# Kernel optimization log

Hardware: AMD Instinct MI355X
Metric: run time of the kernel (lower is better)

Reference implementation:

```python
import jax, jax.numpy as jnp
import numpy as np

B, S, D = 4, 2048, 2048   # batch, seq, embed
E, R = 64, 64             # experts, expert_rank
INIT_SCALE = 0.02


def setup_inputs() -> dict:
    key = jax.random.key(0)
    k_x, k_m, k_up, k_dn = jax.random.split(key, 4)
    x = jax.random.normal(k_x, (B, S, D), dtype=jnp.float32)
    expert_mask = jax.random.uniform(k_m, (B, S, E), dtype=jnp.float32)
    # up_proj weight, out_first=True: [experts, rank, embed]
    w_up = jax.random.normal(k_up, (E, R, D), dtype=jnp.float32) * INIT_SCALE
    # down_proj weight, out_first=True: [embed, experts, rank]
    w_down = jax.random.normal(k_dn, (D, E, R), dtype=jnp.float32) * INIT_SCALE
    return {"x": x, "expert_mask": expert_mask, "w_up": w_up, "w_down": w_down}


def reference(x, expert_mask, w_up, w_down):
    # up projection: [B,S,D] x [E,R,D] -> [B,S,E,R]
    h = jnp.einsum("bsd,erd->bser", x, w_up)
    h = jax.nn.silu(h)
    # mask inactive experts (broadcast over rank)
    h = h * expert_mask[:, :, :, None]
    # down projection: [B,S,E,R] x [D,E,R] -> [B,S,D]
    out = jnp.einsum("bser,der->bsd", h, w_down)
    return out
```

## Files before the change

### kernel.cpp

```cpp
#include <hip/hip_runtime.h>
#include <hip/hip_bf16.h>

typedef unsigned short u16;
typedef unsigned int   u32;
typedef __attribute__((ext_vector_type(8))) short  s16x8;
typedef __attribute__((ext_vector_type(4))) float  f32x4;
typedef __attribute__((ext_vector_type(4))) unsigned short u16x4;

#define MT    8192
#define DE    2048
#define NEXP  64
#define ERDIM 4096

__device__ __forceinline__ u16 to_bf16(float f) {
  u32 u = __builtin_bit_cast(u32, f);
  u32 r = u + 0x7fffu + ((u >> 16) & 1u);
  return (u16)(r >> 16);
}

__global__ void cvt_f32_bf16(const float* __restrict__ in, u16* __restrict__ out, int n) {
  const int stride = gridDim.x * blockDim.x;
  for (int i = blockIdx.x * blockDim.x + threadIdx.x; i * 4 < n; i += stride) {
    const float4 v = *reinterpret_cast<const float4*>(in + (size_t)i * 4);
    u16x4 o;
    o.x = to_bf16(v.x); o.y = to_bf16(v.y); o.z = to_bf16(v.z); o.w = to_bf16(v.w);
    *reinterpret_cast<u16x4*>(out + (size_t)i * 4) = o;
  }
}

#define GLDS(gp, lp) __builtin_amdgcn_global_load_lds(                        \
    (const __attribute__((address_space(1))) void*)(gp),                      \
    (__attribute__((address_space(3))) void*)(lp), 16, 0, 0)

#define BAR() do { asm volatile("" ::: "memory");                             \
                   __builtin_amdgcn_s_barrier();                              \
                   asm volatile("" ::: "memory"); } while (0)

template<int FUSE, int K>
__global__ __launch_bounds__(512, 4) void gemm_bt(
    const u16* __restrict__ A, const u16* __restrict__ Bm,
    const float* __restrict__ mask, void* __restrict__ Cout,
    const int M, const int N)
{
  constexpr int BM = 256, BN = 128, BK = 32;
  constexpr int NT = K / BK;
  constexpr int SLOT = 12288;
  __shared__ __align__(16) u16 lds[3 * SLOT];

  const int nbn = N / BN;
  const int nwg = (int)gridDim.x;
  const int cpx = nwg >> 3;
  const int bid = (int)blockIdx.x;
  const int swz = (bid & 7) * cpx + (bid >> 3);
  const int bm = (swz / nbn) * BM;
  const int bn = (swz % nbn) * BN;

  const int tid  = (int)threadIdx.x;
  const int lane = tid & 63;
  const int w    = tid >> 6;
  const int wr   = w >> 1;
  const int wc   = w & 1;

  const int fr = lane & 15;
  const int cp = (lane >> 4) ^ ((lane >> 1) & 3);

  const int r0 = w * 16 + (lane >> 2);
  const int cl = (lane & 3) ^ ((lane >> 3) & 3);
  const u16* aS0 = A  + (size_t)(bm + r0) * K + cl * 8;
  const u16* aS1 = A  + (size_t)(bm + r0 + 128) * K + cl * 8;
  const u16* bS0 = Bm + (size_t)(bn + r0) * K + cl * 8;
  const int d0 = w * 512;

  f32x4 acc[4][4] = {};

#pragma unroll
  for (int t = 0; t < 2; ++t) {
    u16* dst = lds + t * SLOT;
    GLDS(aS0 + t * BK, dst +        d0);
    GLDS(aS1 + t * BK, dst + 4096 + d0);
    GLDS(bS0 + t * BK, dst + 8192 + d0);
  }
  asm volatile("s_waitcnt vmcnt(3)" ::: "memory");
  BAR();

  int ro = 0;
  int so = 2 * SLOT;
#pragma unroll 3
  for (int t = 0; t < NT; ++t) {
    const u16* sA = lds + ro;
    const u16* sB = lds + ro + 8192;

    s16x8 afr[4], bfr[4];
#pragma unroll
    for (int m = 0; m < 4; ++m)
      afr[m] = *reinterpret_cast<const s16x8*>(
          &sA[(wr * 64 + m * 16 + fr) * 32 + cp * 8]);
#pragma unroll
    for (int n = 0; n < 4; ++n)
      bfr[n] = *reinterpret_cast<const s16x8*>(
          &sB[(wc * 64 + n * 16 + fr) * 32 + cp * 8]);

    if (t + 2 < NT) {
      u16* dst = lds + so;
      const size_t koff = (size_t)(t + 2) * BK;
      GLDS(aS0 + koff, dst +        d0);
      GLDS(aS1 + koff, dst + 4096 + d0);
      GLDS(bS0 + koff, dst + 8192 + d0);
    }

    __builtin_amdgcn_s_setprio(1);
#pragma unroll
    for (int m = 0; m < 4; ++m)
#pragma unroll
      for (int n = 0; n < 4; ++n)
        acc[m][n] = __builtin_amdgcn_mfma_f32_16x16x32_bf16(
            afr[m], bfr[n], acc[m][n], 0, 0, 0);
    __builtin_amdgcn_s_setprio(0);

    if (t + 2 < NT)      asm volatile("s_waitcnt vmcnt(3)" ::: "memory");
    else if (t + 1 < NT) asm volatile("s_waitcnt vmcnt(0)" ::: "memory");

    if (t + 1 < NT) BAR();

    ro = (ro == 2 * SLOT) ? 0 : ro + SLOT;
    so = (so == 2 * SLOT) ? 0 : so + SLOT;
  }

  const int rgrp = (lane >> 4) * 4;
  if (FUSE) {
    u16* H = (u16*)Cout;
    const int ew = (bn + wc * 64) >> 6;
#pragma unroll
    for (int m = 0; m < 4; ++m) {
#pragma unroll
      for (int j = 0; j < 4; ++j) {
        const int grow = bm + wr * 64 + m * 16 + rgrp + j;
        const float mv = mask[(size_t)grow * NEXP + ew];
#pragma unroll
        for (int n = 0; n < 4; ++n) {
          const int gcol = bn + wc * 64 + n * 16 + fr;
          float v = acc[m][n][j];
          v = v / (1.0f + __expf(-v));
          H[(size_t)grow * N + gcol] = to_bf16(v * mv);
        }
      }
    }
  } else {
    float* O = (float*)Cout;
#pragma unroll
    for (int m = 0; m < 4; ++m) {
#pragma unroll
      for (int j = 0; j < 4; ++j) {
        const int grow = bm + wr * 64 + m * 16 + rgrp + j;
#pragma unroll
        for (int n = 0; n < 4; ++n) {
          const int gcol = bn + wc * 64 + n * 16 + fr;
          O[(size_t)grow * N + gcol] = acc[m][n][j];
        }
      }
    }
  }
}

extern "C" void kernel_launch(void* const* d_in, const int* in_sizes, int n_in,
                              void* d_out, int out_size, void* d_ws, size_t ws_size,
                              hipStream_t stream) {
  const float* x     = (const float*)d_in[0];
  const float* emask = (const float*)d_in[1];
  const float* w_up  = (const float*)d_in[2];
  const float* w_dn  = (const float*)d_in[3];
  float* out = (float*)d_out;

  const size_t need = ((size_t)MT * DE + (size_t)ERDIM * DE + (size_t)DE * ERDIM +
                       (size_t)MT * ERDIM) * sizeof(u16);
  if (ws_size < need) return;

  u16* xb  = (u16*)d_ws;
  u16* wub = xb  + (size_t)MT * DE;
  u16* wdb = wub + (size_t)ERDIM * DE;
  u16* hb  = wdb + (size_t)DE * ERDIM;

  hipLaunchKernelGGL(cvt_f32_bf16, dim3(2048), dim3(256), 0, stream, x,    xb,  MT * DE);
  hipLaunchKernelGGL(cvt_f32_bf16, dim3(1024), dim3(256), 0, stream, w_up, wub, ERDIM * DE);
  hipLaunchKernelGGL(cvt_f32_bf16, dim3(1024), dim3(256), 0, stream, w_dn, wdb, DE * ERDIM);

  hipLaunchKernelGGL((gemm_bt<1, DE>), dim3((MT / 256) * (ERDIM / 128)), dim3(512), 0, stream,
                     xb, wub, emask, (void*)hb, MT, ERDIM);
  hipLaunchKernelGGL((gemm_bt<0, ERDIM>), dim3((MT / 256) * (DE / 128)), dim3(512), 0, stream,
                     hb, wdb, nullptr, (void*)out, MT, DE);
}
```

Baseline: 311.2 us.

## Enlarge GEMM tiles to 256x256 with 1024 threads and 4-stage LDS pipeline

```diff
diff --git a/kernel.cpp b/kernel.cpp
--- a/kernel.cpp
+++ b/kernel.cpp
@@ -18,14 +18,23 @@
   return (u16)(r >> 16);
 }
 
-__global__ void cvt_f32_bf16(const float* __restrict__ in, u16* __restrict__ out, int n) {
+__global__ void cvt_all(const float* __restrict__ x,  u16* __restrict__ xo,
+                        const float* __restrict__ wu, u16* __restrict__ wuo,
+                        const float* __restrict__ wd, u16* __restrict__ wdo) {
   const int stride = gridDim.x * blockDim.x;
-  for (int i = blockIdx.x * blockDim.x + threadIdx.x; i * 4 < n; i += stride) {
-    const float4 v = *reinterpret_cast<const float4*>(in + (size_t)i * 4);
-    u16x4 o;
-    o.x = to_bf16(v.x); o.y = to_bf16(v.y); o.z = to_bf16(v.z); o.w = to_bf16(v.w);
-    *reinterpret_cast<u16x4*>(out + (size_t)i * 4) = o;
+  const int t0 = blockIdx.x * blockDim.x + threadIdx.x;
+#define CVT_LOOP(src, dst, nq)                                                \
+  for (int i = t0; i < (nq); i += stride) {                                   \
+    const float4 v = *reinterpret_cast<const float4*>((src) + (size_t)i * 4); \
+    u16x4 o;                                                                  \
+    o.x = to_bf16(v.x); o.y = to_bf16(v.y);                                   \
+    o.z = to_bf16(v.z); o.w = to_bf16(v.w);                                   \
+    *reinterpret_cast<u16x4*>((dst) + (size_t)i * 4) = o;                     \
   }
+  CVT_LOOP(x,  xo,  (MT * DE) / 4)
+  CVT_LOOP(wu, wuo, (ERDIM * DE) / 4)
+  CVT_LOOP(wd, wdo, (DE * ERDIM) / 4)
+#undef CVT_LOOP
 }
 
 #define GLDS(gp, lp) __builtin_amdgcn_global_load_lds(                        \
@@ -37,76 +46,68 @@
                    asm volatile("" ::: "memory"); } while (0)
 
 template<int FUSE, int K>
-__global__ __launch_bounds__(512, 4) void gemm_bt(
+__global__ __launch_bounds__(1024, 4) void gemm_bt(
     const u16* __restrict__ A, const u16* __restrict__ Bm,
     const float* __restrict__ mask, void* __restrict__ Cout,
     const int M, const int N)
 {
-  constexpr int BM = 256, BN = 128, BK = 32;
+  constexpr int BK = 32;
   constexpr int NT = K / BK;
-  constexpr int SLOT = 12288;
-  __shared__ __align__(16) u16 lds[3 * SLOT];
+  constexpr int SLOT = 16384;
+  __shared__ __align__(16) u16 lds[4 * SLOT];
 
-  const int nbn = N / BN;
+  const int nbn = N / 256;
   const int nwg = (int)gridDim.x;
   const int cpx = nwg >> 3;
   const int bid = (int)blockIdx.x;
   const int swz = (bid & 7) * cpx + (bid >> 3);
-  const int bm = (swz / nbn) * BM;
-  const int bn = (swz % nbn) * BN;
+  const int bm = (swz / nbn) * 256;
+  const int bn = (swz % nbn) * 256;
 
   const int tid  = (int)threadIdx.x;
   const int lane = tid & 63;
   const int w    = tid >> 6;
-  const int wr   = w >> 1;
-  const int wc   = w & 1;
+  const int wr   = w >> 2;
+  const int wc   = w & 3;
 
   const int fr = lane & 15;
-  const int cp = (lane >> 4) ^ ((lane >> 1) & 3);
+  const int hi = lane >> 4;
+  const int rdc = fr * 32 + ((hi ^ ((fr >> 1) & 3)) * 8);
 
-  const int r0 = w * 16 + (lane >> 2);
-  const int cl = (lane & 3) ^ ((lane >> 3) & 3);
-  const u16* aS0 = A  + (size_t)(bm + r0) * K + cl * 8;
-  const u16* aS1 = A  + (size_t)(bm + r0 + 128) * K + cl * 8;
-  const u16* bS0 = Bm + (size_t)(bn + r0) * K + cl * 8;
-  const int d0 = w * 512;
+  const int srow = tid >> 2;
+  const int sq   = (tid & 3) ^ ((srow >> 1) & 3);
+  const u16* aS = A  + (size_t)(bm + srow) * K + sq * 8;
+  const u16* bS = Bm + (size_t)(bn + srow) * K + sq * 8;
+
+#define STG_TILE(T, s) do {                                                   \
+    u16* dst = lds + (s) * SLOT;                                              \
+    const size_t ko = (size_t)(T) * BK;                                       \
+    GLDS(aS + ko, dst +        tid * 8);                                      \
+    GLDS(bS + ko, dst + 8192 + tid * 8);                                      \
+  } while (0)
 
   f32x4 acc[4][4] = {};
 
-#pragma unroll
-  for (int t = 0; t < 2; ++t) {
-    u16* dst = lds + t * SLOT;
-    GLDS(aS0 + t * BK, dst +        d0);
-    GLDS(aS1 + t * BK, dst + 4096 + d0);
-    GLDS(bS0 + t * BK, dst + 8192 + d0);
-  }
-  asm volatile("s_waitcnt vmcnt(3)" ::: "memory");
+  STG_TILE(0, 0);
+  STG_TILE(1, 1);
+  STG_TILE(2, 2);
+  asm volatile("s_waitcnt vmcnt(4)" ::: "memory");
   BAR();
 
-  int ro = 0;
-  int so = 2 * SLOT;
-#pragma unroll 3
+#pragma unroll 4
   for (int t = 0; t < NT; ++t) {
-    const u16* sA = lds + ro;
-    const u16* sB = lds + ro + 8192;
+    const u16* sA = lds + (t & 3) * SLOT;
+    const u16* sB = sA + 8192;
 
-    s16x8 afr[4], bfr[4];
+    s16x8 af[4], bf[4];
 #pragma unroll
     for (int m = 0; m < 4; ++m)
-      afr[m] = *reinterpret_cast<const s16x8*>(
-          &sA[(wr * 64 + m * 16 + fr) * 32 + cp * 8]);
+      af[m] = *reinterpret_cast<const s16x8*>(&sA[(wr * 64 + m * 16) * 32 + rdc]);
 #pragma unroll
     for (int n = 0; n < 4; ++n)
-      bfr[n] = *reinterpret_cast<const s16x8*>(
-          &sB[(wc * 64 + n * 16 + fr) * 32 + cp * 8]);
+      bf[n] = *reinterpret_cast<const s16x8*>(&sB[(wc * 64 + n * 16) * 32 + rdc]);
 
-    if (t + 2 < NT) {
-      u16* dst = lds + so;
-      const size_t koff = (size_t)(t + 2) * BK;
-      GLDS(aS0 + koff, dst +        d0);
-      GLDS(aS1 + koff, dst + 4096 + d0);
-      GLDS(bS0 + koff, dst + 8192 + d0);
-    }
+    if (t + 3 < NT) STG_TILE(t + 3, (t + 3) & 3);
 
     __builtin_amdgcn_s_setprio(1);
 #pragma unroll
@@ -114,19 +115,18 @@
 #pragma unroll
       for (int n = 0; n < 4; ++n)
         acc[m][n] = __builtin_amdgcn_mfma_f32_16x16x32_bf16(
-            afr[m], bfr[n], acc[m][n], 0, 0, 0);
+            af[m], bf[n], acc[m][n], 0, 0, 0);
     __builtin_amdgcn_s_setprio(0);
 
-    if (t + 2 < NT)      asm volatile("s_waitcnt vmcnt(3)" ::: "memory");
+    if (t + 3 < NT)      asm volatile("s_waitcnt vmcnt(4)" ::: "memory");
+    else if (t + 2 < NT) asm volatile("s_waitcnt vmcnt(2)" ::: "memory");
     else if (t + 1 < NT) asm volatile("s_waitcnt vmcnt(0)" ::: "memory");
 
     if (t + 1 < NT) BAR();
+  }
+#undef STG_TILE
 
-    ro = (ro == 2 * SLOT) ? 0 : ro + SLOT;
-    so = (so == 2 * SLOT) ? 0 : so + SLOT;
-  }
-
-  const int rgrp = (lane >> 4) * 4;
+  const int rgrp = hi * 4;
   if (FUSE) {
     u16* H = (u16*)Cout;
     const int ew = (bn + wc * 64) >> 6;
@@ -180,12 +180,11 @@
   u16* wdb = wub + (size_t)ERDIM * DE;
   u16* hb  = wdb + (size_t)DE * ERDIM;
 
-  hipLaunchKernelGGL(cvt_f32_bf16, dim3(2048), dim3(256), 0, stream, x,    xb,  MT * DE);
-  hipLaunchKernelGGL(cvt_f32_bf16, dim3(1024), dim3(256), 0, stream, w_up, wub, ERDIM * DE);
-  hipLaunchKernelGGL(cvt_f32_bf16, dim3(1024), dim3(256), 0, stream, w_dn, wdb, DE * ERDIM);
+  hipLaunchKernelGGL(cvt_all, dim3(2048), dim3(256), 0, stream,
+                     x, xb, w_up, wub, w_dn, wdb);
 
-  hipLaunchKernelGGL((gemm_bt<1, DE>), dim3((MT / 256) * (ERDIM / 128)), dim3(512), 0, stream,
+  hipLaunchKernelGGL((gemm_bt<1, DE>), dim3((MT / 256) * (ERDIM / 256)), dim3(1024), 0, stream,
                      xb, wub, emask, (void*)hb, MT, ERDIM);
-  hipLaunchKernelGGL((gemm_bt<0, ERDIM>), dim3((MT / 256) * (DE / 128)), dim3(512), 0, stream,
+  hipLaunchKernelGGL((gemm_bt<0, ERDIM>), dim3((MT / 256) * (DE / 256)), dim3(1024), 0, stream,
                      hb, wdb, nullptr, (void*)out, MT, DE);
 }
```

Measured after the change: 449.5 us. 1.44x slower.
